# Kernel tuning notes

Hardware: AMD Instinct MI355X
Metric: run time of the kernel (lower is better)

## Reference

```python
import jax, jax.numpy as jnp
import numpy as np

N_NODES = 50000
N_EDGES = 800000
N_FEAT = 128
DIM = 64
N_GRAPHS = 512


def setup_inputs() -> dict:
    key = jax.random.key(0)
    k1, k2, k3, k4, k5, k6 = jax.random.split(key, 6)
    x = jax.random.normal(k1, (N_NODES, N_FEAT), dtype=jnp.float32)
    edge_index = jax.random.randint(k2, (2, N_EDGES), 0, N_NODES, dtype=jnp.int64)
    batch = jnp.sort(jax.random.randint(k3, (N_NODES,), 0, N_GRAPHS, dtype=jnp.int64))
    W1 = jax.random.normal(k4, (N_FEAT, DIM), dtype=jnp.float32) * 0.05
    W2 = jax.random.normal(k5, (DIM, DIM), dtype=jnp.float32) * 0.05
    Wfc = jax.random.normal(k6, (DIM, 1), dtype=jnp.float32) * 0.05
    return {"x": x, "edge_index": edge_index, "batch": batch,
            "W1": W1, "W2": W2, "Wfc": Wfc}


def _gcn_conv(h, src, dst, W):
    # GCNConv(normalize=False, bias=False): linear transform then scatter-add
    # over edges: out[dst] += (h @ W)[src]
    h = jnp.einsum('nf,fd->nd', h, W)
    return jax.ops.segment_sum(h[src], dst, num_segments=N_NODES)


def reference(x, edge_index, batch, W1, W2, Wfc):
    src, dst = edge_index[0], edge_index[1]
    h = jax.nn.relu(_gcn_conv(x, src, dst, W1))          # [N, DIM]
    h = _gcn_conv(h, src, dst, W2)                        # [N, DIM]
    # global_mean_pool over graph ids
    counts = jax.ops.segment_sum(jnp.ones((N_NODES,), h.dtype), batch,
                                 num_segments=N_GRAPHS)   # [G]
    pooled = jax.ops.segment_sum(h, batch, num_segments=N_GRAPHS)
    pooled = pooled / jnp.maximum(counts, 1.0)[:, None]   # [G, DIM]
    return jax.nn.sigmoid(pooled @ Wfc)                   # [G, 1]
```

## Files before the change

kernel.cpp:

```cpp
#include <hip/hip_runtime.h>
#include <cmath>

#define N_NODES 50000
#define N_EDGES 800000
#define N_FEAT 128
#define DIM 64
#define N_GRAPHS 512
#define GGRID ((N_NODES + 63) / 64)
#define NBKT GGRID
#define BH_BLK 128
#define EPB (N_EDGES / BH_BLK)
#define NCNT (NBKT * BH_BLK)
#define P2_NBLK ((NCNT + 511) / 512)
#define BKT_CAP 2048

typedef short short8 __attribute__((ext_vector_type(8)));
typedef float floatx4 __attribute__((ext_vector_type(4)));

__device__ __forceinline__ unsigned short f2bf(float f) {
  union { float f; unsigned int u; } v; v.f = f;
  return (unsigned short)((v.u + 0x7FFFu + ((v.u >> 16) & 1u)) >> 16);
}
__device__ __forceinline__ float bf2f(unsigned short u) {
  union { unsigned int u; float f; } v; v.u = (unsigned int)u << 16;
  return v.f;
}

__global__ __launch_bounds__(256) void bhist_w2fc(const int* __restrict__ dst,
                                                  int* __restrict__ cnt,
                                                  const float* __restrict__ W2,
                                                  const float* __restrict__ Wfc,
                                                  float* __restrict__ w2fc,
                                                  const float* __restrict__ W1,
                                                  unsigned short* __restrict__ w1sh,
                                                  unsigned short* __restrict__ w1sl) {
  if (blockIdx.x == BH_BLK) {
    int k = threadIdx.x;
    if (k < 64) {
      float s = 0.f;
#pragma unroll 8
      for (int j = 0; j < 64; j++) s += W2[k * 64 + j] * Wfc[j];
      w2fc[k] = s;
    }
    return;
  }
  if (blockIdx.x == BH_BLK + 1) {
    int tid = threadIdx.x;
#pragma unroll
    for (int i = 0; i < 32; i++) {
      int idx = i * 256 + tid;
      int kk = idx & 127, c = idx >> 7;
      float f = W1[kk * 64 + c];
      unsigned short h = f2bf(f);
      unsigned short l = f2bf(f - bf2f(h));
      w1sh[idx] = h;
      w1sl[idx] = l;
    }
    return;
  }
  __shared__ int lh[NBKT];
  const int tid = threadIdx.x, k = blockIdx.x;
  for (int i = tid; i < NBKT; i += 256) lh[i] = 0;
  __syncthreads();
  const int base = k * EPB;
  for (int j = tid; j < EPB; j += 256)
    atomicAdd(&lh[dst[base + j] >> 6], 1);
  __syncthreads();
  for (int i = tid; i < NBKT; i += 256) cnt[i * BH_BLK + k] = lh[i];
}

__global__ __launch_bounds__(256) void f_psum(const int* __restrict__ cnt,
                                              int* __restrict__ partials) {
  __shared__ int ws[4];
  const int tid = threadIdx.x;
  const int2* cnt2 = (const int2*)cnt;
  int idx = blockIdx.x * 256 + tid;
  int v = 0;
  if (idx * 2 < NCNT) { int2 c = cnt2[idx]; v = c.x + c.y; }
#pragma unroll
  for (int off = 32; off; off >>= 1) v += __shfl_down(v, off, 64);
  int lane = tid & 63, w = tid >> 6;
  if (lane == 0) ws[w] = v;
  __syncthreads();
  if (tid == 0) partials[blockIdx.x] = ws[0] + ws[1] + ws[2] + ws[3];
}

__global__ __launch_bounds__(256) void f_sblocks(int* __restrict__ cnt,
                                                 const int* __restrict__ partials,
                                                 int* __restrict__ bucket_ptr) {
  __shared__ int buf[256];
  __shared__ int pbuf[256];
  const int tid = threadIdx.x;
  int2* cnt2 = (int2*)cnt;
  const int idx = blockIdx.x * 256 + tid;
  int2 c = make_int2(0, 0);
  if (idx * 2 < NCNT) c = cnt2[idx];
  int s = c.x + c.y;
  buf[tid] = s;
  pbuf[tid] = (tid < P2_NBLK) ? partials[tid] : 0;
  __syncthreads();
  for (int off = 1; off < 256; off <<= 1) {
    int t1 = (tid >= off) ? buf[tid - off] : 0;
    int t2 = (tid >= off) ? pbuf[tid - off] : 0;
    __syncthreads();
    buf[tid] += t1;
    pbuf[tid] += t2;
    __syncthreads();
  }
  const int thr_excl = buf[tid] - s;
  const int base = (blockIdx.x > 0) ? pbuf[blockIdx.x - 1] : 0;
  if (idx * 2 < NCNT) {
    int e0 = base + thr_excl;
    cnt2[idx] = make_int2(e0, e0 + c.x);
    int p = idx * 2;
    if ((p & (BH_BLK - 1)) == 0) bucket_ptr[p >> 7] = e0;
    if (p + 1 == NCNT - 1) bucket_ptr[NBKT] = e0 + c.x + c.y;
  }
}

__device__ __forceinline__ void gemm1_mfma(const float* __restrict__ x,
                                           const unsigned short* __restrict__ w1sh,
                                           const unsigned short* __restrict__ w1sl,
                                           unsigned short* __restrict__ h1,
                                           int row0, int tid) {
  const int lane = tid & 63, w = tid >> 6;
  const int g = lane >> 4, c15 = lane & 15;
  const int ra = row0 + (w << 4) + c15;
  const bool va = ra < N_NODES;
  const float* xr = &x[(size_t)(va ? ra : 0) * N_FEAT];
  floatx4 acc[4];
#pragma unroll
  for (int i = 0; i < 4; i++) acc[i] = (floatx4){0.f, 0.f, 0.f, 0.f};

#pragma unroll
  for (int kb = 0; kb < 128; kb += 32) {
    const int ka = kb + g * 8;
    float4 v0 = make_float4(0.f, 0.f, 0.f, 0.f), v1 = v0;
    if (va) {
      v0 = *(const float4*)&xr[ka];
      v1 = *(const float4*)&xr[ka + 4];
    }
    const float fv[8] = {v0.x, v0.y, v0.z, v0.w, v1.x, v1.y, v1.z, v1.w};
    short8 ah, al;
#pragma unroll
    for (int j = 0; j < 8; j++) {
      unsigned short h = f2bf(fv[j]);
      ah[j] = (short)h;
      al[j] = (short)f2bf(fv[j] - bf2f(h));
    }
#pragma unroll
    for (int ct = 0; ct < 4; ct++) {
      const int cb = ct * 16 + c15;
      short8 bh = *(const short8*)&w1sh[cb * 128 + ka];
      short8 bl = *(const short8*)&w1sl[cb * 128 + ka];
      acc[ct] = __builtin_amdgcn_mfma_f32_16x16x32_bf16(ah, bh, acc[ct], 0, 0, 0);
      acc[ct] = __builtin_amdgcn_mfma_f32_16x16x32_bf16(ah, bl, acc[ct], 0, 0, 0);
      acc[ct] = __builtin_amdgcn_mfma_f32_16x16x32_bf16(al, bh, acc[ct], 0, 0, 0);
    }
  }

#pragma unroll
  for (int ct = 0; ct < 4; ct++) {
#pragma unroll
    for (int r = 0; r < 4; r++) {
      int gr = row0 + (w << 4) + (g << 2) + r;
      if (gr < N_NODES) h1[(size_t)gr * 64 + ct * 16 + c15] = f2bf(acc[ct][r]);
    }
  }
}

__global__ __launch_bounds__(256) void gemm1_bscatter(
    const float* __restrict__ x,
    const unsigned short* __restrict__ w1sh,
    const unsigned short* __restrict__ w1sl,
    unsigned short* __restrict__ h1, const int* __restrict__ src,
    const int* __restrict__ dst, const int* __restrict__ cnt,
    unsigned int* __restrict__ ebuf) {
  __shared__ int loff[NBKT];
  const int tid = threadIdx.x;
  if (blockIdx.x >= BH_BLK) {
    gemm1_mfma(x, w1sh, w1sl, h1, (blockIdx.x - BH_BLK) * 64, tid);
  } else {
    const int k = blockIdx.x;
    for (int i = tid; i < NBKT; i += 256) loff[i] = cnt[i * BH_BLK + k];
    __syncthreads();
    const int base = k * EPB;
    for (int j = tid; j < EPB; j += 256) {
      int e = base + j;
      int d = dst[e];
      int pos = atomicAdd(&loff[d >> 6], 1);
      ebuf[pos] = ((unsigned int)src[e] << 6) | (unsigned int)(d & 63);
    }
  }
}

__global__ __launch_bounds__(1024, 8) void gather_z_fused(
    const unsigned short* __restrict__ h1,
    const unsigned int* __restrict__ ebuf,
    const int* __restrict__ bucket_ptr,
    const float* __restrict__ w2fc,
    float* __restrict__ z) {
  __shared__ int colL[BKT_CAP];
  __shared__ int lstart[64];
  __shared__ int lcur[64];
  __shared__ float sw[64];
  const int tid = threadIdx.x;
  const int b = blockIdx.x;
  const int p0 = bucket_ptr[b];
  int cnt = bucket_ptr[b + 1] - p0;
  if (cnt > BKT_CAP) cnt = BKT_CAP;

  if (tid < 64) { lstart[tid] = 0; sw[tid] = w2fc[tid]; }
  __syncthreads();
  for (int i = tid; i < cnt; i += 1024)
    atomicAdd(&lstart[ebuf[p0 + i] & 63], 1);
  __syncthreads();
  if (tid < 64) {
    int v = lstart[tid], s = v;
#pragma unroll
    for (int off = 1; off < 64; off <<= 1) {
      int t = __shfl_up(s, off, 64);
      if (tid >= off) s += t;
    }
    lstart[tid] = s - v;
    lcur[tid] = s - v;
  }
  __syncthreads();
  for (int i = tid; i < cnt; i += 1024) {
    unsigned int u = ebuf[p0 + i];
    int pos = atomicAdd(&lcur[u & 63], 1);
    colL[pos] = (int)(u >> 6);
  }
  __syncthreads();

  const int lane = tid & 63, w = tid >> 6;
  const int eo = lane >> 4, qfo = (lane & 15) << 2;
#pragma unroll
  for (int ni = 0; ni < 4; ni++) {
    const int r = ni * 16 + w;
    const int i1 = lcur[r];
    int i = lstart[r];
    float4 acc = make_float4(0.f, 0.f, 0.f, 0.f);
    for (; i + 16 <= i1; i += 16) {
      int s0 = colL[i + eo];
      int s1 = colL[i + 4 + eo];
      int s2 = colL[i + 8 + eo];
      int s3 = colL[i + 12 + eo];
      ushort4 u0 = *(const ushort4*)&h1[(size_t)s0 * 64 + qfo];
      ushort4 u1 = *(const ushort4*)&h1[(size_t)s1 * 64 + qfo];
      ushort4 u2 = *(const ushort4*)&h1[(size_t)s2 * 64 + qfo];
      ushort4 u3 = *(const ushort4*)&h1[(size_t)s3 * 64 + qfo];
      acc.x += (bf2f(u0.x) + bf2f(u1.x)) + (bf2f(u2.x) + bf2f(u3.x));
      acc.y += (bf2f(u0.y) + bf2f(u1.y)) + (bf2f(u2.y) + bf2f(u3.y));
      acc.z += (bf2f(u0.z) + bf2f(u1.z)) + (bf2f(u2.z) + bf2f(u3.z));
      acc.w += (bf2f(u0.w) + bf2f(u1.w)) + (bf2f(u2.w) + bf2f(u3.w));
    }
    for (; i + 4 <= i1; i += 4) {
      int s = colL[i + eo];
      ushort4 u = *(const ushort4*)&h1[(size_t)s * 64 + qfo];
      acc.x += bf2f(u.x); acc.y += bf2f(u.y);
      acc.z += bf2f(u.z); acc.w += bf2f(u.w);
    }
    if (eo < i1 - i) {
      int s = colL[i + eo];
      ushort4 u = *(const ushort4*)&h1[(size_t)s * 64 + qfo];
      acc.x += bf2f(u.x); acc.y += bf2f(u.y);
      acc.z += bf2f(u.z); acc.w += bf2f(u.w);
    }
#pragma unroll
    for (int m = 16; m <= 32; m <<= 1) {
      acc.x += __shfl_xor(acc.x, m, 64);
      acc.y += __shfl_xor(acc.y, m, 64);
      acc.z += __shfl_xor(acc.z, m, 64);
      acc.w += __shfl_xor(acc.w, m, 64);
    }
    float p = fmaxf(acc.x, 0.f) * sw[qfo] + fmaxf(acc.y, 0.f) * sw[qfo + 1] +
              fmaxf(acc.z, 0.f) * sw[qfo + 2] + fmaxf(acc.w, 0.f) * sw[qfo + 3];
#pragma unroll
    for (int m = 1; m <= 8; m <<= 1) p += __shfl_xor(p, m, 64);
    int node = b * 64 + r;
    if (lane == 0 && node < N_NODES) z[node] = p;
  }
}

__global__ __launch_bounds__(256) void graph_pool(const float* __restrict__ z,
                                                  const unsigned int* __restrict__ ebuf,
                                                  const int* __restrict__ bucket_ptr,
                                                  const int* __restrict__ batch,
                                                  float* __restrict__ out) {
  __shared__ float sacc[4];
  int g = blockIdx.x;
  int tid = threadIdx.x, lane = tid & 63, w = tid >> 6;

  int lo = 0, hi = N_NODES;
  while (lo < hi) { int mid = (lo + hi) >> 1; if (batch[mid] < g) lo = mid + 1; else hi = mid; }
  const int start = lo;
  hi = N_NODES;
  while (lo < hi) { int mid = (lo + hi) >> 1; if (batch[mid] < g + 1) lo = mid + 1; else hi = mid; }
  const int end = lo;

  float s = 0.f;
  if (end > start) {
    const int b0 = start >> 6, b1 = ((end - 1) >> 6) + 1;
    for (int b = b0; b < b1; b++) {
      const int q0 = bucket_ptr[b], q1 = bucket_ptr[b + 1];
      const int base = b << 6;
      for (int i = q0 + tid; i < q1; i += 256) {
        unsigned int u = ebuf[i];
        int d = base + (int)(u & 63);
        if (d >= start && d < end) s += z[u >> 6];
      }
    }
  }
#pragma unroll
  for (int off = 32; off; off >>= 1) s += __shfl_down(s, off, 64);
  if (lane == 0) sacc[w] = s;
  __syncthreads();
  if (tid == 0) {
    float v = sacc[0] + sacc[1] + sacc[2] + sacc[3];
    v /= fmaxf((float)(end - start), 1.f);
    out[g] = 1.f / (1.f + expf(-v));
  }
}

extern "C" void kernel_launch(void* const* d_in, const int* in_sizes, int n_in,
                              void* d_out, int out_size, void* d_ws, size_t ws_size,
                              hipStream_t stream) {
  const float* x     = (const float*)d_in[0];
  const int*   ei    = (const int*)d_in[1];
  const int*   batch = (const int*)d_in[2];
  const float* W1    = (const float*)d_in[3];
  const float* W2    = (const float*)d_in[4];
  const float* Wfc   = (const float*)d_in[5];
  float*       out   = (float*)d_out;

  const int* src = ei;
  const int* dst = ei + N_EDGES;

  char* ws = (char*)d_ws;
  unsigned short* h1 = (unsigned short*)(ws);
  unsigned short* w1sh = (unsigned short*)(ws + (size_t)N_NODES * DIM * 2);
  unsigned short* w1sl = w1sh + N_FEAT * DIM;
  float* z    = (float*)(w1sl + N_FEAT * DIM);
  float* w2fc = z + N_NODES;
  int*   cnt  = (int*)(w2fc + 64);
  int*   partials = cnt + NCNT;
  unsigned int* ebuf = (unsigned int*)(partials + P2_NBLK);
  int*   bucket_ptr  = (int*)(ebuf + N_EDGES);

  bhist_w2fc<<<BH_BLK + 2, 256, 0, stream>>>(dst, cnt, W2, Wfc, w2fc,
                                             W1, w1sh, w1sl);
  f_psum<<<P2_NBLK, 256, 0, stream>>>(cnt, partials);
  f_sblocks<<<P2_NBLK, 256, 0, stream>>>(cnt, partials, bucket_ptr);

  gemm1_bscatter<<<GGRID + BH_BLK, 256, 0, stream>>>(x, w1sh, w1sl, h1, src,
                                                     dst, cnt, ebuf);

  gather_z_fused<<<NBKT, 1024, 0, stream>>>(h1, ebuf, bucket_ptr, w2fc, z);

  graph_pool<<<N_GRAPHS, 256, 0, stream>>>(z, ebuf, bucket_ptr, batch, out);
}
```

Before: 153.9 us.

## Replace bucketed per-block histogram with per-node CSR built by global atomics

```diff
diff --git a/kernel.cpp b/kernel.cpp
--- a/kernel.cpp
+++ b/kernel.cpp
@@ -7,12 +7,10 @@
 #define DIM 64
 #define N_GRAPHS 512
 #define GGRID ((N_NODES + 63) / 64)
-#define NBKT GGRID
 #define BH_BLK 128
 #define EPB (N_EDGES / BH_BLK)
-#define NCNT (NBKT * BH_BLK)
-#define P2_NBLK ((NCNT + 511) / 512)
-#define BKT_CAP 2048
+#define NND_PAD 50176
+#define P2_NBLK (NND_PAD / 512)
 
 typedef short short8 __attribute__((ext_vector_type(8)));
 typedef float floatx4 __attribute__((ext_vector_type(4)));
@@ -27,7 +25,7 @@
 }
 
 __global__ __launch_bounds__(256) void bhist_w2fc(const int* __restrict__ dst,
-                                                  int* __restrict__ cnt,
+                                                  int* __restrict__ indeg,
                                                   const float* __restrict__ W2,
                                                   const float* __restrict__ Wfc,
                                                   float* __restrict__ w2fc,
@@ -58,25 +56,20 @@
     }
     return;
   }
-  __shared__ int lh[NBKT];
   const int tid = threadIdx.x, k = blockIdx.x;
-  for (int i = tid; i < NBKT; i += 256) lh[i] = 0;
-  __syncthreads();
   const int base = k * EPB;
   for (int j = tid; j < EPB; j += 256)
-    atomicAdd(&lh[dst[base + j] >> 6], 1);
-  __syncthreads();
-  for (int i = tid; i < NBKT; i += 256) cnt[i * BH_BLK + k] = lh[i];
-}
-
-__global__ __launch_bounds__(256) void f_psum(const int* __restrict__ cnt,
+    atomicAdd(&indeg[dst[base + j]], 1);
+}
+
+__global__ __launch_bounds__(256) void f_psum(const int* __restrict__ indeg,
                                               int* __restrict__ partials) {
   __shared__ int ws[4];
   const int tid = threadIdx.x;
-  const int2* cnt2 = (const int2*)cnt;
+  const int2* c2 = (const int2*)indeg;
   int idx = blockIdx.x * 256 + tid;
   int v = 0;
-  if (idx * 2 < NCNT) { int2 c = cnt2[idx]; v = c.x + c.y; }
+  if (idx * 2 < NND_PAD) { int2 c = c2[idx]; v = c.x + c.y; }
 #pragma unroll
   for (int off = 32; off; off >>= 1) v += __shfl_down(v, off, 64);
   int lane = tid & 63, w = tid >> 6;
@@ -85,16 +78,17 @@
   if (tid == 0) partials[blockIdx.x] = ws[0] + ws[1] + ws[2] + ws[3];
 }
 
-__global__ __launch_bounds__(256) void f_sblocks(int* __restrict__ cnt,
+__global__ __launch_bounds__(256) void f_sblocks(const int* __restrict__ indeg,
                                                  const int* __restrict__ partials,
-                                                 int* __restrict__ bucket_ptr) {
+                                                 int* __restrict__ rp,
+                                                 int* __restrict__ rc) {
   __shared__ int buf[256];
   __shared__ int pbuf[256];
   const int tid = threadIdx.x;
-  int2* cnt2 = (int2*)cnt;
+  const int2* c2 = (const int2*)indeg;
   const int idx = blockIdx.x * 256 + tid;
   int2 c = make_int2(0, 0);
-  if (idx * 2 < NCNT) c = cnt2[idx];
+  if (idx * 2 < NND_PAD) c = c2[idx];
   int s = c.x + c.y;
   buf[tid] = s;
   pbuf[tid] = (tid < P2_NBLK) ? partials[tid] : 0;
@@ -109,12 +103,11 @@
   }
   const int thr_excl = buf[tid] - s;
   const int base = (blockIdx.x > 0) ? pbuf[blockIdx.x - 1] : 0;
-  if (idx * 2 < NCNT) {
+  if (idx * 2 < NND_PAD) {
     int e0 = base + thr_excl;
-    cnt2[idx] = make_int2(e0, e0 + c.x);
-    int p = idx * 2;
-    if ((p & (BH_BLK - 1)) == 0) bucket_ptr[p >> 7] = e0;
-    if (p + 1 == NCNT - 1) bucket_ptr[NBKT] = e0 + c.x + c.y;
+    int2 o = make_int2(e0, e0 + c.x);
+    ((int2*)rp)[idx] = o;
+    ((int2*)rc)[idx] = o;
   }
 }
 
@@ -174,22 +167,18 @@
     const unsigned short* __restrict__ w1sh,
     const unsigned short* __restrict__ w1sl,
     unsigned short* __restrict__ h1, const int* __restrict__ src,
-    const int* __restrict__ dst, const int* __restrict__ cnt,
+    const int* __restrict__ dst, int* __restrict__ rc,
     unsigned int* __restrict__ ebuf) {
-  __shared__ int loff[NBKT];
   const int tid = threadIdx.x;
   if (blockIdx.x >= BH_BLK) {
     gemm1_mfma(x, w1sh, w1sl, h1, (blockIdx.x - BH_BLK) * 64, tid);
   } else {
-    const int k = blockIdx.x;
-    for (int i = tid; i < NBKT; i += 256) loff[i] = cnt[i * BH_BLK + k];
-    __syncthreads();
-    const int base = k * EPB;
+    const int base = blockIdx.x * EPB;
     for (int j = tid; j < EPB; j += 256) {
       int e = base + j;
       int d = dst[e];
-      int pos = atomicAdd(&loff[d >> 6], 1);
-      ebuf[pos] = ((unsigned int)src[e] << 6) | (unsigned int)(d & 63);
+      int pos = atomicAdd(&rc[d], 1);
+      ebuf[pos] = (unsigned int)src[e];
     }
   }
 }
@@ -197,40 +186,15 @@
 __global__ __launch_bounds__(1024, 8) void gather_z_fused(
     const unsigned short* __restrict__ h1,
     const unsigned int* __restrict__ ebuf,
-    const int* __restrict__ bucket_ptr,
+    const int* __restrict__ rp,
     const float* __restrict__ w2fc,
     float* __restrict__ z) {
-  __shared__ int colL[BKT_CAP];
-  __shared__ int lstart[64];
-  __shared__ int lcur[64];
+  __shared__ int srp[65];
   __shared__ float sw[64];
   const int tid = threadIdx.x;
   const int b = blockIdx.x;
-  const int p0 = bucket_ptr[b];
-  int cnt = bucket_ptr[b + 1] - p0;
-  if (cnt > BKT_CAP) cnt = BKT_CAP;
-
-  if (tid < 64) { lstart[tid] = 0; sw[tid] = w2fc[tid]; }
-  __syncthreads();
-  for (int i = tid; i < cnt; i += 1024)
-    atomicAdd(&lstart[ebuf[p0 + i] & 63], 1);
-  __syncthreads();
-  if (tid < 64) {
-    int v = lstart[tid], s = v;
-#pragma unroll
-    for (int off = 1; off < 64; off <<= 1) {
-      int t = __shfl_up(s, off, 64);
-      if (tid >= off) s += t;
-    }
-    lstart[tid] = s - v;
-    lcur[tid] = s - v;
-  }
-  __syncthreads();
-  for (int i = tid; i < cnt; i += 1024) {
-    unsigned int u = ebuf[p0 + i];
-    int pos = atomicAdd(&lcur[u & 63], 1);
-    colL[pos] = (int)(u >> 6);
-  }
+  if (tid < 65) srp[tid] = rp[b * 64 + tid];
+  if (tid < 64) sw[tid] = w2fc[tid];
   __syncthreads();
 
   const int lane = tid & 63, w = tid >> 6;
@@ -238,14 +202,14 @@
 #pragma unroll
   for (int ni = 0; ni < 4; ni++) {
     const int r = ni * 16 + w;
-    const int i1 = lcur[r];
-    int i = lstart[r];
+    const int i1 = srp[r + 1];
+    int i = srp[r];
     float4 acc = make_float4(0.f, 0.f, 0.f, 0.f);
     for (; i + 16 <= i1; i += 16) {
-      int s0 = colL[i + eo];
-      int s1 = colL[i + 4 + eo];
-      int s2 = colL[i + 8 + eo];
-      int s3 = colL[i + 12 + eo];
+      int s0 = ebuf[i + eo];
+      int s1 = ebuf[i + 4 + eo];
+      int s2 = ebuf[i + 8 + eo];
+      int s3 = ebuf[i + 12 + eo];
       ushort4 u0 = *(const ushort4*)&h1[(size_t)s0 * 64 + qfo];
       ushort4 u1 = *(const ushort4*)&h1[(size_t)s1 * 64 + qfo];
       ushort4 u2 = *(const ushort4*)&h1[(size_t)s2 * 64 + qfo];
@@ -256,13 +220,13 @@
       acc.w += (bf2f(u0.w) + bf2f(u1.w)) + (bf2f(u2.w) + bf2f(u3.w));
     }
     for (; i + 4 <= i1; i += 4) {
-      int s = colL[i + eo];
+      int s = ebuf[i + eo];
       ushort4 u = *(const ushort4*)&h1[(size_t)s * 64 + qfo];
       acc.x += bf2f(u.x); acc.y += bf2f(u.y);
       acc.z += bf2f(u.z); acc.w += bf2f(u.w);
     }
     if (eo < i1 - i) {
-      int s = colL[i + eo];
+      int s = ebuf[i + eo];
       ushort4 u = *(const ushort4*)&h1[(size_t)s * 64 + qfo];
       acc.x += bf2f(u.x); acc.y += bf2f(u.y);
       acc.z += bf2f(u.z); acc.w += bf2f(u.w);
@@ -285,7 +249,7 @@
 
 __global__ __launch_bounds__(256) void graph_pool(const float* __restrict__ z,
                                                   const unsigned int* __restrict__ ebuf,
-                                                  const int* __restrict__ bucket_ptr,
+                                                  const int* __restrict__ rp,
                                                   const int* __restrict__ batch,
                                                   float* __restrict__ out) {
   __shared__ float sacc[4];
@@ -299,19 +263,9 @@
   while (lo < hi) { int mid = (lo + hi) >> 1; if (batch[mid] < g + 1) lo = mid + 1; else hi = mid; }
   const int end = lo;
 
+  const int e0 = rp[start], e1 = rp[end];
   float s = 0.f;
-  if (end > start) {
-    const int b0 = start >> 6, b1 = ((end - 1) >> 6) + 1;
-    for (int b = b0; b < b1; b++) {
-      const int q0 = bucket_ptr[b], q1 = bucket_ptr[b + 1];
-      const int base = b << 6;
-      for (int i = q0 + tid; i < q1; i += 256) {
-        unsigned int u = ebuf[i];
-        int d = base + (int)(u & 63);
-        if (d >= start && d < end) s += z[u >> 6];
-      }
-    }
-  }
+  for (int i = e0 + tid; i < e1; i += 256) s += z[ebuf[i]];
 #pragma unroll
   for (int off = 32; off; off >>= 1) s += __shfl_down(s, off, 64);
   if (lane == 0) sacc[w] = s;
@@ -343,20 +297,22 @@
   unsigned short* w1sl = w1sh + N_FEAT * DIM;
   float* z    = (float*)(w1sl + N_FEAT * DIM);
   float* w2fc = z + N_NODES;
-  int*   cnt  = (int*)(w2fc + 64);
-  int*   partials = cnt + NCNT;
-  unsigned int* ebuf = (unsigned int*)(partials + P2_NBLK);
-  int*   bucket_ptr  = (int*)(ebuf + N_EDGES);
-
-  bhist_w2fc<<<BH_BLK + 2, 256, 0, stream>>>(dst, cnt, W2, Wfc, w2fc,
+  int*   indeg = (int*)(w2fc + 64);
+  int*   rp    = indeg + NND_PAD;
+  int*   rc    = rp + NND_PAD;
+  int*   partials = rc + NND_PAD;
+  unsigned int* ebuf = (unsigned int*)(partials + 128);
+
+  hipMemsetAsync(indeg, 0, NND_PAD * sizeof(int), stream);
+  bhist_w2fc<<<BH_BLK + 2, 256, 0, stream>>>(dst, indeg, W2, Wfc, w2fc,
                                              W1, w1sh, w1sl);
-  f_psum<<<P2_NBLK, 256, 0, stream>>>(cnt, partials);
-  f_sblocks<<<P2_NBLK, 256, 0, stream>>>(cnt, partials, bucket_ptr);
+  f_psum<<<P2_NBLK, 256, 0, stream>>>(indeg, partials);
+  f_sblocks<<<P2_NBLK, 256, 0, stream>>>(indeg, partials, rp, rc);
 
   gemm1_bscatter<<<GGRID + BH_BLK, 256, 0, stream>>>(x, w1sh, w1sl, h1, src,
-                                                     dst, cnt, ebuf);
-
-  gather_z_fused<<<NBKT, 1024, 0, stream>>>(h1, ebuf, bucket_ptr, w2fc, z);
-
-  graph_pool<<<N_GRAPHS, 256, 0, stream>>>(z, ebuf, bucket_ptr, batch, out);
-}
+                                                     dst, rc, ebuf);
+
+  gather_z_fused<<<GGRID, 1024, 0, stream>>>(h1, ebuf, rp, w2fc, z);
+
+  graph_pool<<<N_GRAPHS, 256, 0, stream>>>(z, ebuf, rp, batch, out);
+}
```

New measurement: 205.7 us. 1.34x slower.
